# Performance work log

Hardware: AMD Instinct MI355X
Metric: run time of the kernel (lower is better)

Reference implementation:

```python
import jax, jax.numpy as jnp
import numpy as np

MIN_STD = 0.01
FOURIER_SCALE = 20.0


def _grid_sample_bilinear(h_flat, gx, gy):
    """Bilinear grid_sample with align_corners=True.
    h_flat: (N, C, H, W); gx, gy: (N, P) in [-1, 1].
    Returns (N, P, C)."""
    N, C, H, W = h_flat.shape
    x = (gx + 1.0) * 0.5 * (W - 1)
    y = (gy + 1.0) * 0.5 * (H - 1)
    x0 = jnp.clip(jnp.floor(x), 0, W - 1)
    y0 = jnp.clip(jnp.floor(y), 0, H - 1)
    x1 = jnp.clip(x0 + 1, 0, W - 1)
    y1 = jnp.clip(y0 + 1, 0, H - 1)
    wx = x - x0
    wy = y - y0
    x0i, x1i = x0.astype(jnp.int32), x1.astype(jnp.int32)
    y0i, y1i = y0.astype(jnp.int32), y1.astype(jnp.int32)
    hf = h_flat.reshape(N, C, H * W)  # flatten spatial for gather

    def gather(yi, xi):
        idx = (yi * W + xi)[:, None, :]  # (N,1,P)
        return jnp.take_along_axis(hf, idx, axis=2)  # (N,C,P)

    v00 = gather(y0i, x0i)
    v01 = gather(y0i, x1i)
    v10 = gather(y1i, x0i)
    v11 = gather(y1i, x1i)
    wx_ = wx[:, None, :]
    wy_ = wy[:, None, :]
    top = v00 * (1 - wx_) + v01 * wx_
    bot = v10 * (1 - wx_) + v11 * wx_
    out = top * (1 - wy_) + bot * wy_  # (N,C,P)
    return out.transpose(0, 2, 1)  # (N,P,C)


def setup_inputs() -> dict:
    key = jax.random.key(0)
    ks = jax.random.split(key, 9)
    B, T, C, Hg, Wg, P = 8, 16, 128, 64, 64, 2048
    h_dim, fmap = 128, 128
    in_dim = h_dim + 2 * fmap  # 384
    h_grid = jax.random.normal(ks[0], (B, T, C, Hg, Wg), dtype=jnp.float32)
    xs = jax.random.uniform(ks[1], (B, T, P, 1), dtype=jnp.float32)
    ys = jax.random.uniform(ks[2], (B, T, P, 1), dtype=jnp.float32)
    B_mat = jax.random.normal(ks[3], (2, fmap), dtype=jnp.float32) * FOURIER_SCALE
    W0 = jax.random.normal(ks[4], (in_dim, h_dim), dtype=jnp.float32) / np.sqrt(in_dim)
    b0 = jnp.zeros((h_dim,), dtype=jnp.float32)
    W1 = jax.random.normal(ks[5], (h_dim, h_dim), dtype=jnp.float32) / np.sqrt(h_dim)
    b1 = jnp.zeros((h_dim,), dtype=jnp.float32)
    W2 = jax.random.normal(ks[6], (h_dim, 2), dtype=jnp.float32) / np.sqrt(h_dim)
    b2 = jnp.zeros((2,), dtype=jnp.float32)
    return {"h_grid": h_grid, "xs": xs, "ys": ys, "B_mat": B_mat,
            "W0": W0, "b0": b0, "W1": W1, "b1": b1, "W2": W2, "b2": b2}


def reference(h_grid, xs, ys, B_mat, W0, b0, W1, b1, W2, b2):
    B, T, P, _ = xs.shape
    _, _, C, Hg, Wg = h_grid.shape
    h_flat = h_grid.reshape(B * T, C, Hg, Wg)
    coords = jnp.concatenate([xs, ys], axis=-1).reshape(B * T, P, 2)
    # map [spatial_min, spatial_max]=[0,1] to [-1,1]
    g = 2.0 * coords - 1.0
    sampled = _grid_sample_bilinear(h_flat, g[..., 0], g[..., 1])  # (BT,P,C)
    # Fourier features: [sin(2pi x B), cos(2pi x B)]
    proj = 2.0 * jnp.pi * jnp.einsum('npd,df->npf', coords, B_mat)
    spatial = jnp.concatenate([jnp.sin(proj), jnp.cos(proj)], axis=-1)  # (BT,P,256)
    x = jnp.concatenate([sampled, spatial], axis=-1)  # (BT,P,384)
    x = jax.nn.relu(x @ W0 + b0)
    x = jax.nn.relu(x @ W1 + b1)
    out = (x @ W2 + b2).reshape(B, T, P, 2)
    mu = out[..., 0:1]
    sigma = jax.nn.softplus(out[..., 1:2]) + MIN_STD
    return jnp.concatenate([mu, sigma], axis=-1)  # (B,T,P,2)
```

## Files before the change

kernel.cpp:

```cpp
#include <hip/hip_runtime.h>
#include <hip/hip_bf16.h>
#include <math.h>

typedef __attribute__((ext_vector_type(8))) short short8;
typedef __attribute__((ext_vector_type(4))) float f32x4;

__device__ __forceinline__ float b2f(unsigned short u) {
    union { unsigned int i; float f; } v; v.i = ((unsigned int)u) << 16; return v.f;
}
__device__ __forceinline__ unsigned short f2b(float f) {
    __hip_bfloat16 h = __float2bfloat16(f);
    return *reinterpret_cast<unsigned short*>(&h);
}

__global__ __launch_bounds__(256) void transpose_h(const float* __restrict__ hg,
                                                   unsigned short* __restrict__ ht) {
    __shared__ float t[64][65];
    int bid = blockIdx.x;
    int n  = bid >> 7;
    int cb = (bid >> 6) & 1;
    int pb = bid & 63;
    int tid = threadIdx.x;
    int j = tid & 63, i0 = tid >> 6;
    const float* src = hg + ((size_t)(n * 128 + cb * 64)) * 4096 + pb * 64;
#pragma unroll
    for (int ii = 0; ii < 16; ++ii) {
        int i = i0 + ii * 4;
        t[i][j] = src[(size_t)i * 4096 + j];
    }
    __syncthreads();
    int c = tid & 63, j0 = tid >> 6;
    unsigned short* dst = ht + ((size_t)n * 4096 + pb * 64) * 128 + cb * 64 + c;
#pragma unroll
    for (int jj = 0; jj < 16; ++jj) {
        int jr = j0 + jj * 4;
        dst[(size_t)jr * 128] = f2b(t[c][jr]);
    }
}

__global__ void prep_weights(const float* __restrict__ W0, const float* __restrict__ W1,
                             unsigned short* __restrict__ w0t, unsigned short* __restrict__ w1t) {
    int i = blockIdx.x * 256 + threadIdx.x;
    const int total0 = 128 * 384, total1 = 128 * 128;
    for (int idx = i; idx < total0; idx += gridDim.x * 256) {
        int j = idx / 384, k = idx - j * 384;
        w0t[idx] = f2b(W0[k * 128 + j]);
    }
    for (int idx = i; idx < total1; idx += gridDim.x * 256) {
        int j = idx >> 7, k = idx & 127;
        w1t[idx] = f2b(W1[k * 128 + j]);
    }
}

#define HSTR 136
#define MFMA_BF16 __builtin_amdgcn_mfma_f32_16x16x32_bf16

__device__ __forceinline__ const short8* w0frag(const unsigned short* w0s, int row, int kb) {
    return (const short8*)((const char*)w0s + row * 768 + (kb ^ ((row & 7) << 4)));
}

__global__ __launch_bounds__(512, 2) void fused_decoder(
    const unsigned short* __restrict__ ht,
    const float* __restrict__ xs, const float* __restrict__ ys,
    const float* __restrict__ Bm,
    const unsigned short* __restrict__ w0t, const float* __restrict__ b0,
    const unsigned short* __restrict__ w1t, const float* __restrict__ b1,
    const float* __restrict__ W2, const float* __restrict__ b2,
    float* __restrict__ out)
{
    __shared__ unsigned short w0s[128 * 384];
    __shared__ unsigned short hb_all[8 * 16 * HSTR];
    __shared__ unsigned short w2l[256];

    int tid = threadIdx.x, lane = tid & 63, w = tid >> 6;
    int lr = lane & 15, lg = lane >> 4;
    unsigned short* hb = hb_all + w * 16 * HSTR;

    {
        const short8* src = (const short8*)w0t;
#pragma unroll
        for (int it = 0; it < 12; ++it) {
            int c = tid + it * 512;
            int row = c / 48;
            int wb = (c - row * 48) * 16;
            short8 v = src[c];
            *(short8*)((char*)w0s + row * 768 + (wb ^ ((row & 7) << 4))) = v;
        }
        if (tid < 256) { int o = tid >> 7, k = tid & 127; w2l[o * 128 + k] = f2b(W2[k * 2 + o]); }
    }
    __syncthreads();

    int bid = blockIdx.x;
    int swz = (bid & 7) * 128 + (bid >> 3);
    int n = swz >> 3;
    int pbw = (swz & 7) * 256 + w * 32;
    int gp0 = n * 2048 + pbw;

    float xm[2], ym[2], wxv[2], wyv[2];
    int o00[2], o01[2], o10[2], o11[2];
#pragma unroll
    for (int m = 0; m < 2; ++m) {
        int gp = gp0 + m * 16 + lr;
        float x = xs[gp], y = ys[gp];
        xm[m] = x; ym[m] = y;
        float px = x * 63.f, py = y * 63.f;
        float x0f = fminf(fmaxf(floorf(px), 0.f), 63.f);
        float y0f = fminf(fmaxf(floorf(py), 0.f), 63.f);
        wxv[m] = px - x0f; wyv[m] = py - y0f;
        int xi0 = (int)x0f, yi0 = (int)y0f;
        int xi1 = min(xi0 + 1, 63), yi1 = min(yi0 + 1, 63);
        o00[m] = (yi0 * 64 + xi0) * 256;
        o01[m] = (yi0 * 64 + xi1) * 256;
        o10[m] = (yi1 * 64 + xi0) * 256;
        o11[m] = (yi1 * 64 + xi1) * 256;
    }
    const char* base = (const char*)ht + ((size_t)n << 20) + lg * 16;

    f32x4 acc[2][8];
#pragma unroll
    for (int nj = 0; nj < 8; ++nj) {
        float bv = b0[nj * 16 + lr];
        acc[0][nj] = (f32x4){bv, bv, bv, bv};
        acc[1][nj] = acc[0][nj];
    }

    short8 c00[2], c01[2], c10[2], c11[2];
#pragma unroll
    for (int m = 0; m < 2; ++m) {
        c00[m] = *(const short8*)(base + o00[m]);
        c01[m] = *(const short8*)(base + o01[m]);
        c10[m] = *(const short8*)(base + o10[m]);
        c11[m] = *(const short8*)(base + o11[m]);
    }

#pragma unroll
    for (int s = 0; s < 4; ++s) {
        int f0 = s * 32 + lg * 8;
        f32x4 B0a = *(const f32x4*)&Bm[f0];
        f32x4 B0b = *(const f32x4*)&Bm[f0 + 4];
        f32x4 B1a = *(const f32x4*)&Bm[128 + f0];
        f32x4 B1b = *(const f32x4*)&Bm[128 + f0 + 4];
        short8 asn[2], acs[2];
#pragma unroll
        for (int m = 0; m < 2; ++m) {
            float t_[8];
#pragma unroll
            for (int j = 0; j < 4; ++j) {
                t_[j]     = xm[m] * B0a[j] + ym[m] * B1a[j];
                t_[4 + j] = xm[m] * B0b[j] + ym[m] * B1b[j];
            }
#pragma unroll
            for (int j = 0; j < 8; ++j) {
                float tf = t_[j] - floorf(t_[j]);
                float sv, cv;
                asm("v_sin_f32 %0, %1" : "=v"(sv) : "v"(tf));
                asm("v_cos_f32 %0, %1" : "=v"(cv) : "v"(tf));
                asn[m][j] = (short)f2b(sv);
                acs[m][j] = (short)f2b(cv);
            }
        }
        int kbs = (4 + s) * 64 + lg * 16, kbc = (8 + s) * 64 + lg * 16;
#pragma unroll
        for (int nj = 0; nj < 8; ++nj) {
            short8 bs = *w0frag(w0s, nj * 16 + lr, kbs);
            acc[0][nj] = MFMA_BF16(asn[0], bs, acc[0][nj], 0, 0, 0);
            acc[1][nj] = MFMA_BF16(asn[1], bs, acc[1][nj], 0, 0, 0);
        }
#pragma unroll
        for (int nj = 0; nj < 8; ++nj) {
            short8 bc = *w0frag(w0s, nj * 16 + lr, kbc);
            acc[0][nj] = MFMA_BF16(acs[0], bc, acc[0][nj], 0, 0, 0);
            acc[1][nj] = MFMA_BF16(acs[1], bc, acc[1][nj], 0, 0, 0);
        }

        short8 a[2];
#pragma unroll
        for (int m = 0; m < 2; ++m) {
            float wx = wxv[m], wy = wyv[m];
            float ivx = 1.f - wx, ivy = 1.f - wy;
#pragma unroll
            for (int j = 0; j < 8; ++j) {
                float top = b2f((unsigned short)c00[m][j]) * ivx + b2f((unsigned short)c01[m][j]) * wx;
                float bot = b2f((unsigned short)c10[m][j]) * ivx + b2f((unsigned short)c11[m][j]) * wx;
                a[m][j] = (short)f2b(top * ivy + bot * wy);
            }
        }
        if (s < 3) {
            int so = (s + 1) * 64;
#pragma unroll
            for (int m = 0; m < 2; ++m) {
                c00[m] = *(const short8*)(base + o00[m] + so);
                c01[m] = *(const short8*)(base + o01[m] + so);
                c10[m] = *(const short8*)(base + o10[m] + so);
                c11[m] = *(const short8*)(base + o11[m] + so);
            }
        }
        int kba = s * 64 + lg * 16;
#pragma unroll
        for (int nj = 0; nj < 8; ++nj) {
            short8 b = *w0frag(w0s, nj * 16 + lr, kba);
            acc[0][nj] = MFMA_BF16(a[0], b, acc[0][nj], 0, 0, 0);
            acc[1][nj] = MFMA_BF16(a[1], b, acc[1][nj], 0, 0, 0);
        }
    }

    short8 a1[2][4];
#pragma unroll
    for (int m = 0; m < 2; ++m) {
#pragma unroll
        for (int nj = 0; nj < 8; ++nj)
#pragma unroll
            for (int r = 0; r < 4; ++r)
                hb[(lg * 4 + r) * HSTR + nj * 16 + lr] = f2b(fmaxf(acc[m][nj][r], 0.f));
        asm volatile("s_waitcnt lgkmcnt(0)" ::: "memory");
#pragma unroll
        for (int ks = 0; ks < 4; ++ks)
            a1[m][ks] = *(const short8*)&hb[lr * HSTR + ks * 32 + lg * 8];
        asm volatile("s_waitcnt lgkmcnt(0)" ::: "memory");
    }
#pragma unroll
    for (int nj = 0; nj < 8; ++nj) {
        float bv = b1[nj * 16 + lr];
        acc[0][nj] = (f32x4){bv, bv, bv, bv};
        acc[1][nj] = acc[0][nj];
    }
#pragma unroll
    for (int ks = 0; ks < 4; ++ks)
#pragma unroll
        for (int nj = 0; nj < 8; ++nj) {
            short8 b = *(const short8*)&w1t[(nj * 16 + lr) * 128 + ks * 32 + lg * 8];
            acc[0][nj] = MFMA_BF16(a1[0][ks], b, acc[0][nj], 0, 0, 0);
            acc[1][nj] = MFMA_BF16(a1[1][ks], b, acc[1][nj], 0, 0, 0);
        }

    float bb2 = (lr < 2) ? b2[lr] : 0.f;
#pragma unroll
    for (int m = 0; m < 2; ++m) {
#pragma unroll
        for (int nj = 0; nj < 8; ++nj)
#pragma unroll
            for (int r = 0; r < 4; ++r)
                hb[(lg * 4 + r) * HSTR + nj * 16 + lr] = f2b(fmaxf(acc[m][nj][r], 0.f));
        asm volatile("s_waitcnt lgkmcnt(0)" ::: "memory");
        f32x4 acc2 = (f32x4){bb2, bb2, bb2, bb2};
#pragma unroll
        for (int ks = 0; ks < 4; ++ks) {
            short8 a2 = *(const short8*)&hb[lr * HSTR + ks * 32 + lg * 8];
            short8 bz = (short8){0, 0, 0, 0, 0, 0, 0, 0};
            if (lr < 2) bz = *(const short8*)&w2l[lr * 128 + ks * 32 + lg * 8];
            acc2 = MFMA_BF16(a2, bz, acc2, 0, 0, 0);
        }
        asm volatile("s_waitcnt lgkmcnt(0)" ::: "memory");
        if (lr < 2) {
#pragma unroll
            for (int r = 0; r < 4; ++r) {
                int gp = gp0 + m * 16 + lg * 4 + r;
                float v = acc2[r];
                if (lr == 0) {
                    out[gp * 2] = v;
                } else {
                    float sp = (v > 20.f) ? v : log1pf(expf(v));
                    out[gp * 2 + 1] = sp + 0.01f;
                }
            }
        }
    }
}

extern "C" void kernel_launch(void* const* d_in, const int* in_sizes, int n_in,
                              void* d_out, int out_size, void* d_ws, size_t ws_size,
                              hipStream_t stream) {
    const float* h_grid = (const float*)d_in[0];
    const float* xs = (const float*)d_in[1];
    const float* ys = (const float*)d_in[2];
    const float* Bm = (const float*)d_in[3];
    const float* W0 = (const float*)d_in[4];
    const float* b0 = (const float*)d_in[5];
    const float* W1 = (const float*)d_in[6];
    const float* b1 = (const float*)d_in[7];
    const float* W2 = (const float*)d_in[8];
    const float* b2 = (const float*)d_in[9];
    float* out = (float*)d_out;

    unsigned short* ht  = (unsigned short*)d_ws;
    unsigned short* w0t = (unsigned short*)((char*)d_ws + 134217728ull);
    unsigned short* w1t = w0t + 128 * 384;

    hipLaunchKernelGGL(transpose_h, dim3(16384), dim3(256), 0, stream, h_grid, ht);
    hipLaunchKernelGGL(prep_weights, dim3(64), dim3(256), 0, stream, W0, W1, w0t, w1t);
    hipLaunchKernelGGL(fused_decoder, dim3(1024), dim3(512), 0, stream,
                       ht, xs, ys, Bm, w0t, b0, w1t, b1, W2, b2, out);
}
```

Before: 210.7 us.

## Vectorize transpose stores, pad W0 in LDS, double-buffer grid-sample corner loads

Result: faster. 198.8 us (-5.6%).

```diff
diff --git a/kernel.cpp b/kernel.cpp
--- a/kernel.cpp
+++ b/kernel.cpp
@@ -4,6 +4,7 @@
 
 typedef __attribute__((ext_vector_type(8))) short short8;
 typedef __attribute__((ext_vector_type(4))) float f32x4;
+typedef __attribute__((ext_vector_type(4))) unsigned short us4;
 
 __device__ __forceinline__ float b2f(unsigned short u) {
     union { unsigned int i; float f; } v; v.i = ((unsigned int)u) << 16; return v.f;
@@ -15,33 +16,35 @@
 
 __global__ __launch_bounds__(256) void transpose_h(const float* __restrict__ hg,
                                                    unsigned short* __restrict__ ht) {
-    __shared__ float t[64][65];
+    __shared__ float t[128][65];
     int bid = blockIdx.x;
-    int n  = bid >> 7;
-    int cb = (bid >> 6) & 1;
-    int pb = bid & 63;
+    int n = bid >> 6, pb = bid & 63;
     int tid = threadIdx.x;
+    const float* src = hg + (size_t)n * 128 * 4096 + pb * 64;
     int j = tid & 63, i0 = tid >> 6;
-    const float* src = hg + ((size_t)(n * 128 + cb * 64)) * 4096 + pb * 64;
-#pragma unroll
-    for (int ii = 0; ii < 16; ++ii) {
-        int i = i0 + ii * 4;
-        t[i][j] = src[(size_t)i * 4096 + j];
+#pragma unroll
+    for (int ii = 0; ii < 32; ++ii) {
+        int ch = ii * 4 + i0;
+        t[ch][j] = src[(size_t)ch * 4096 + j];
     }
     __syncthreads();
-    int c = tid & 63, j0 = tid >> 6;
-    unsigned short* dst = ht + ((size_t)n * 4096 + pb * 64) * 128 + cb * 64 + c;
-#pragma unroll
-    for (int jj = 0; jj < 16; ++jj) {
-        int jr = j0 + jj * 4;
-        dst[(size_t)jr * 128] = f2b(t[c][jr]);
+#pragma unroll
+    for (int it = 0; it < 8; ++it) {
+        int idx = tid + it * 256;
+        int px = idx >> 5, cq = idx & 31;
+        us4 o;
+#pragma unroll
+        for (int r = 0; r < 4; ++r) o[r] = f2b(t[cq * 4 + r][px]);
+        *(us4*)&ht[((size_t)n * 4096 + pb * 64 + px) * 128 + cq * 4] = o;
     }
 }
 
 __global__ void prep_weights(const float* __restrict__ W0, const float* __restrict__ W1,
-                             unsigned short* __restrict__ w0t, unsigned short* __restrict__ w1t) {
+                             const float* __restrict__ W2,
+                             unsigned short* __restrict__ w0t, unsigned short* __restrict__ w1t,
+                             unsigned short* __restrict__ w2p) {
     int i = blockIdx.x * 256 + threadIdx.x;
-    const int total0 = 128 * 384, total1 = 128 * 128;
+    const int total0 = 128 * 384, total1 = 128 * 128, total2 = 16 * 128;
     for (int idx = i; idx < total0; idx += gridDim.x * 256) {
         int j = idx / 384, k = idx - j * 384;
         w0t[idx] = f2b(W0[k * 128 + j]);
@@ -50,14 +53,15 @@
         int j = idx >> 7, k = idx & 127;
         w1t[idx] = f2b(W1[k * 128 + j]);
     }
-}
-
-#define HSTR 136
+    for (int idx = i; idx < total2; idx += gridDim.x * 256) {
+        int r = idx >> 7, k = idx & 127;
+        w2p[idx] = (r < 2) ? f2b(W2[k * 2 + r]) : (unsigned short)0;
+    }
+}
+
+#define W0P 784
+#define HBP 272
 #define MFMA_BF16 __builtin_amdgcn_mfma_f32_16x16x32_bf16
-
-__device__ __forceinline__ const short8* w0frag(const unsigned short* w0s, int row, int kb) {
-    return (const short8*)((const char*)w0s + row * 768 + (kb ^ ((row & 7) << 4)));
-}
 
 __global__ __launch_bounds__(512, 2) void fused_decoder(
     const unsigned short* __restrict__ ht,
@@ -65,45 +69,40 @@
     const float* __restrict__ Bm,
     const unsigned short* __restrict__ w0t, const float* __restrict__ b0,
     const unsigned short* __restrict__ w1t, const float* __restrict__ b1,
-    const float* __restrict__ W2, const float* __restrict__ b2,
+    const unsigned short* __restrict__ w2p, const float* __restrict__ b2,
     float* __restrict__ out)
 {
-    __shared__ unsigned short w0s[128 * 384];
-    __shared__ unsigned short hb_all[8 * 16 * HSTR];
-    __shared__ unsigned short w2l[256];
-
+    __shared__ char smem[128 * W0P + 8 * 16 * HBP];
+    char* w0s = smem;
     int tid = threadIdx.x, lane = tid & 63, w = tid >> 6;
     int lr = lane & 15, lg = lane >> 4;
-    unsigned short* hb = hb_all + w * 16 * HSTR;
+    char* hb = smem + 128 * W0P + w * 16 * HBP;
 
     {
         const short8* src = (const short8*)w0t;
-#pragma unroll
+#pragma unroll 1
         for (int it = 0; it < 12; ++it) {
             int c = tid + it * 512;
-            int row = c / 48;
-            int wb = (c - row * 48) * 16;
-            short8 v = src[c];
-            *(short8*)((char*)w0s + row * 768 + (wb ^ ((row & 7) << 4))) = v;
-        }
-        if (tid < 256) { int o = tid >> 7, k = tid & 127; w2l[o * 128 + k] = f2b(W2[k * 2 + o]); }
+            int row = c / 48, cc = c - row * 48;
+            *(short8*)(w0s + row * W0P + cc * 16) = src[c];
+        }
     }
     __syncthreads();
 
     int bid = blockIdx.x;
-    int swz = (bid & 7) * 128 + (bid >> 3);
-    int n = swz >> 3;
-    int pbw = (swz & 7) * 256 + w * 32;
-    int gp0 = n * 2048 + pbw;
+    int x = bid & 7, s = bid >> 3;
+    int n = x * 16 + (s >> 3);
+    int pt = s & 7;
+    int gp0 = n * 2048 + pt * 256 + w * 32;
 
     float xm[2], ym[2], wxv[2], wyv[2];
     int o00[2], o01[2], o10[2], o11[2];
 #pragma unroll
     for (int m = 0; m < 2; ++m) {
         int gp = gp0 + m * 16 + lr;
-        float x = xs[gp], y = ys[gp];
-        xm[m] = x; ym[m] = y;
-        float px = x * 63.f, py = y * 63.f;
+        float xc = xs[gp], yc = ys[gp];
+        xm[m] = xc; ym[m] = yc;
+        float px = xc * 63.f, py = yc * 63.f;
         float x0f = fminf(fmaxf(floorf(px), 0.f), 63.f);
         float y0f = fminf(fmaxf(floorf(py), 0.f), 63.f);
         wxv[m] = px - x0f; wyv[m] = py - y0f;
@@ -124,83 +123,153 @@
         acc[1][nj] = acc[0][nj];
     }
 
-    short8 c00[2], c01[2], c10[2], c11[2];
+    short8 A00[2], A01[2], A10[2], A11[2];
+    short8 B00[2], B01[2], B10[2], B11[2];
 #pragma unroll
     for (int m = 0; m < 2; ++m) {
-        c00[m] = *(const short8*)(base + o00[m]);
-        c01[m] = *(const short8*)(base + o01[m]);
-        c10[m] = *(const short8*)(base + o10[m]);
-        c11[m] = *(const short8*)(base + o11[m]);
-    }
-
-#pragma unroll
-    for (int s = 0; s < 4; ++s) {
-        int f0 = s * 32 + lg * 8;
-        f32x4 B0a = *(const f32x4*)&Bm[f0];
-        f32x4 B0b = *(const f32x4*)&Bm[f0 + 4];
-        f32x4 B1a = *(const f32x4*)&Bm[128 + f0];
-        f32x4 B1b = *(const f32x4*)&Bm[128 + f0 + 4];
-        short8 asn[2], acs[2];
-#pragma unroll
-        for (int m = 0; m < 2; ++m) {
-            float t_[8];
-#pragma unroll
-            for (int j = 0; j < 4; ++j) {
-                t_[j]     = xm[m] * B0a[j] + ym[m] * B1a[j];
-                t_[4 + j] = xm[m] * B0b[j] + ym[m] * B1b[j];
-            }
-#pragma unroll
-            for (int j = 0; j < 8; ++j) {
-                float tf = t_[j] - floorf(t_[j]);
-                float sv, cv;
-                asm("v_sin_f32 %0, %1" : "=v"(sv) : "v"(tf));
-                asm("v_cos_f32 %0, %1" : "=v"(cv) : "v"(tf));
-                asn[m][j] = (short)f2b(sv);
-                acs[m][j] = (short)f2b(cv);
-            }
-        }
-        int kbs = (4 + s) * 64 + lg * 16, kbc = (8 + s) * 64 + lg * 16;
-#pragma unroll
-        for (int nj = 0; nj < 8; ++nj) {
-            short8 bs = *w0frag(w0s, nj * 16 + lr, kbs);
-            acc[0][nj] = MFMA_BF16(asn[0], bs, acc[0][nj], 0, 0, 0);
-            acc[1][nj] = MFMA_BF16(asn[1], bs, acc[1][nj], 0, 0, 0);
-        }
-#pragma unroll
-        for (int nj = 0; nj < 8; ++nj) {
-            short8 bc = *w0frag(w0s, nj * 16 + lr, kbc);
-            acc[0][nj] = MFMA_BF16(acs[0], bc, acc[0][nj], 0, 0, 0);
-            acc[1][nj] = MFMA_BF16(acs[1], bc, acc[1][nj], 0, 0, 0);
-        }
-
-        short8 a[2];
-#pragma unroll
-        for (int m = 0; m < 2; ++m) {
-            float wx = wxv[m], wy = wyv[m];
-            float ivx = 1.f - wx, ivy = 1.f - wy;
-#pragma unroll
-            for (int j = 0; j < 8; ++j) {
-                float top = b2f((unsigned short)c00[m][j]) * ivx + b2f((unsigned short)c01[m][j]) * wx;
-                float bot = b2f((unsigned short)c10[m][j]) * ivx + b2f((unsigned short)c11[m][j]) * wx;
-                a[m][j] = (short)f2b(top * ivy + bot * wy);
-            }
-        }
-        if (s < 3) {
-            int so = (s + 1) * 64;
+        A00[m] = *(const short8*)(base + o00[m]);
+        A01[m] = *(const short8*)(base + o01[m]);
+        A10[m] = *(const short8*)(base + o10[m]);
+        A11[m] = *(const short8*)(base + o11[m]);
+        B00[m] = *(const short8*)(base + o00[m] + 64);
+        B01[m] = *(const short8*)(base + o01[m] + 64);
+        B10[m] = *(const short8*)(base + o10[m] + 64);
+        B11[m] = *(const short8*)(base + o11[m] + 64);
+    }
+
+#pragma unroll 1
+    for (int s2 = 0; s2 < 2; ++s2) {
+        {
+            int q = 2 * s2;
+            short8 asn[2], acs[2];
 #pragma unroll
             for (int m = 0; m < 2; ++m) {
-                c00[m] = *(const short8*)(base + o00[m] + so);
-                c01[m] = *(const short8*)(base + o01[m] + so);
-                c10[m] = *(const short8*)(base + o10[m] + so);
-                c11[m] = *(const short8*)(base + o11[m] + so);
-            }
-        }
-        int kba = s * 64 + lg * 16;
-#pragma unroll
-        for (int nj = 0; nj < 8; ++nj) {
-            short8 b = *w0frag(w0s, nj * 16 + lr, kba);
-            acc[0][nj] = MFMA_BF16(a[0], b, acc[0][nj], 0, 0, 0);
-            acc[1][nj] = MFMA_BF16(a[1], b, acc[1][nj], 0, 0, 0);
+                int f0 = q * 32 + lg * 8;
+                f32x4 B0a = *(const f32x4*)&Bm[f0];
+                f32x4 B0b = *(const f32x4*)&Bm[f0 + 4];
+                f32x4 B1a = *(const f32x4*)&Bm[128 + f0];
+                f32x4 B1b = *(const f32x4*)&Bm[128 + f0 + 4];
+                float t_[8];
+#pragma unroll
+                for (int j = 0; j < 4; ++j) {
+                    t_[j]     = xm[m] * B0a[j] + ym[m] * B1a[j];
+                    t_[4 + j] = xm[m] * B0b[j] + ym[m] * B1b[j];
+                }
+#pragma unroll
+                for (int j = 0; j < 8; ++j) {
+                    float tf = t_[j] - floorf(t_[j]);
+                    float sv, cv;
+                    asm("v_sin_f32 %0, %1" : "=v"(sv) : "v"(tf));
+                    asm("v_cos_f32 %0, %1" : "=v"(cv) : "v"(tf));
+                    asn[m][j] = (short)f2b(sv);
+                    acs[m][j] = (short)f2b(cv);
+                }
+            }
+#pragma unroll
+            for (int nj = 0; nj < 8; ++nj) {
+                short8 bs = *(const short8*)(w0s + (nj * 16 + lr) * W0P + (4 + q) * 64 + lg * 16);
+                acc[0][nj] = MFMA_BF16(asn[0], bs, acc[0][nj], 0, 0, 0);
+                acc[1][nj] = MFMA_BF16(asn[1], bs, acc[1][nj], 0, 0, 0);
+            }
+#pragma unroll
+            for (int nj = 0; nj < 8; ++nj) {
+                short8 bc = *(const short8*)(w0s + (nj * 16 + lr) * W0P + (8 + q) * 64 + lg * 16);
+                acc[0][nj] = MFMA_BF16(acs[0], bc, acc[0][nj], 0, 0, 0);
+                acc[1][nj] = MFMA_BF16(acs[1], bc, acc[1][nj], 0, 0, 0);
+            }
+            short8 a[2];
+#pragma unroll
+            for (int m = 0; m < 2; ++m) {
+                float wx = wxv[m], wy = wyv[m];
+                float ivx = 1.f - wx, ivy = 1.f - wy;
+#pragma unroll
+                for (int j = 0; j < 8; ++j) {
+                    float top = b2f((unsigned short)A00[m][j]) * ivx + b2f((unsigned short)A01[m][j]) * wx;
+                    float bot = b2f((unsigned short)A10[m][j]) * ivx + b2f((unsigned short)A11[m][j]) * wx;
+                    a[m][j] = (short)f2b(top * ivy + bot * wy);
+                }
+            }
+            if (s2 == 0) {
+#pragma unroll
+                for (int m = 0; m < 2; ++m) {
+                    A00[m] = *(const short8*)(base + o00[m] + 128);
+                    A01[m] = *(const short8*)(base + o01[m] + 128);
+                    A10[m] = *(const short8*)(base + o10[m] + 128);
+                    A11[m] = *(const short8*)(base + o11[m] + 128);
+                }
+            }
+#pragma unroll
+            for (int nj = 0; nj < 8; ++nj) {
+                short8 b = *(const short8*)(w0s + (nj * 16 + lr) * W0P + q * 64 + lg * 16);
+                acc[0][nj] = MFMA_BF16(a[0], b, acc[0][nj], 0, 0, 0);
+                acc[1][nj] = MFMA_BF16(a[1], b, acc[1][nj], 0, 0, 0);
+            }
+        }
+        {
+            int q = 2 * s2 + 1;
+            short8 asn[2], acs[2];
+#pragma unroll
+            for (int m = 0; m < 2; ++m) {
+                int f0 = q * 32 + lg * 8;
+                f32x4 B0a = *(const f32x4*)&Bm[f0];
+                f32x4 B0b = *(const f32x4*)&Bm[f0 + 4];
+                f32x4 B1a = *(const f32x4*)&Bm[128 + f0];
+                f32x4 B1b = *(const f32x4*)&Bm[128 + f0 + 4];
+                float t_[8];
+#pragma unroll
+                for (int j = 0; j < 4; ++j) {
+                    t_[j]     = xm[m] * B0a[j] + ym[m] * B1a[j];
+                    t_[4 + j] = xm[m] * B0b[j] + ym[m] * B1b[j];
+                }
+#pragma unroll
+                for (int j = 0; j < 8; ++j) {
+                    float tf = t_[j] - floorf(t_[j]);
+                    float sv, cv;
+                    asm("v_sin_f32 %0, %1" : "=v"(sv) : "v"(tf));
+                    asm("v_cos_f32 %0, %1" : "=v"(cv) : "v"(tf));
+                    asn[m][j] = (short)f2b(sv);
+                    acs[m][j] = (short)f2b(cv);
+                }
+            }
+#pragma unroll
+            for (int nj = 0; nj < 8; ++nj) {
+                short8 bs = *(const short8*)(w0s + (nj * 16 + lr) * W0P + (4 + q) * 64 + lg * 16);
+                acc[0][nj] = MFMA_BF16(asn[0], bs, acc[0][nj], 0, 0, 0);
+                acc[1][nj] = MFMA_BF16(asn[1], bs, acc[1][nj], 0, 0, 0);
+            }
+#pragma unroll
+            for (int nj = 0; nj < 8; ++nj) {
+                short8 bc = *(const short8*)(w0s + (nj * 16 + lr) * W0P + (8 + q) * 64 + lg * 16);
+                acc[0][nj] = MFMA_BF16(acs[0], bc, acc[0][nj], 0, 0, 0);
+                acc[1][nj] = MFMA_BF16(acs[1], bc, acc[1][nj], 0, 0, 0);
+            }
+            short8 a[2];
+#pragma unroll
+            for (int m = 0; m < 2; ++m) {
+                float wx = wxv[m], wy = wyv[m];
+                float ivx = 1.f - wx, ivy = 1.f - wy;
+#pragma unroll
+                for (int j = 0; j < 8; ++j) {
+                    float top = b2f((unsigned short)B00[m][j]) * ivx + b2f((unsigned short)B01[m][j]) * wx;
+                    float bot = b2f((unsigned short)B10[m][j]) * ivx + b2f((unsigned short)B11[m][j]) * wx;
+                    a[m][j] = (short)f2b(top * ivy + bot * wy);
+                }
+            }
+            if (s2 == 0) {
+#pragma unroll
+                for (int m = 0; m < 2; ++m) {
+                    B00[m] = *(const short8*)(base + o00[m] + 192);
+                    B01[m] = *(const short8*)(base + o01[m] + 192);
+                    B10[m] = *(const short8*)(base + o10[m] + 192);
+                    B11[m] = *(const short8*)(base + o11[m] + 192);
+                }
+            }
+#pragma unroll
+            for (int nj = 0; nj < 8; ++nj) {
+                short8 b = *(const short8*)(w0s + (nj * 16 + lr) * W0P + q * 64 + lg * 16);
+                acc[0][nj] = MFMA_BF16(a[0], b, acc[0][nj], 0, 0, 0);
+                acc[1][nj] = MFMA_BF16(a[1], b, acc[1][nj], 0, 0, 0);
+            }
         }
     }
 
@@ -210,12 +279,15 @@
 #pragma unroll
         for (int nj = 0; nj < 8; ++nj)
 #pragma unroll
-            for (int r = 0; r < 4; ++r)
-                hb[(lg * 4 + r) * HSTR + nj * 16 + lr] = f2b(fmaxf(acc[m][nj][r], 0.f));
+            for (int r = 0; r < 4; ++r) {
+                int row = lg * 4 + r;
+                *(unsigned short*)(hb + row * HBP + (nj * 16 + lr) * 2) =
+                    f2b(fmaxf(acc[m][nj][r], 0.f));
+            }
         asm volatile("s_waitcnt lgkmcnt(0)" ::: "memory");
 #pragma unroll
         for (int ks = 0; ks < 4; ++ks)
-            a1[m][ks] = *(const short8*)&hb[lr * HSTR + ks * 32 + lg * 8];
+            a1[m][ks] = *(const short8*)(hb + lr * HBP + ks * 64 + lg * 16);
         asm volatile("s_waitcnt lgkmcnt(0)" ::: "memory");
     }
 #pragma unroll
@@ -239,28 +311,30 @@
 #pragma unroll
         for (int nj = 0; nj < 8; ++nj)
 #pragma unroll
-            for (int r = 0; r < 4; ++r)
-                hb[(lg * 4 + r) * HSTR + nj * 16 + lr] = f2b(fmaxf(acc[m][nj][r], 0.f));
+            for (int r = 0; r < 4; ++r) {
+                int row = lg * 4 + r;
+                *(unsigned short*)(hb + row * HBP + (nj * 16 + lr) * 2) =
+                    f2b(fmaxf(acc[m][nj][r], 0.f));
+            }
         asm volatile("s_waitcnt lgkmcnt(0)" ::: "memory");
         f32x4 acc2 = (f32x4){bb2, bb2, bb2, bb2};
 #pragma unroll
         for (int ks = 0; ks < 4; ++ks) {
-            short8 a2 = *(const short8*)&hb[lr * HSTR + ks * 32 + lg * 8];
-            short8 bz = (short8){0, 0, 0, 0, 0, 0, 0, 0};
-            if (lr < 2) bz = *(const short8*)&w2l[lr * 128 + ks * 32 + lg * 8];
+            short8 a2 = *(const short8*)(hb + lr * HBP + ks * 64 + lg * 16);
+            short8 bz = *(const short8*)&w2p[lr * 128 + ks * 32 + lg * 8];
             acc2 = MFMA_BF16(a2, bz, acc2, 0, 0, 0);
         }
         asm volatile("s_waitcnt lgkmcnt(0)" ::: "memory");
         if (lr < 2) {
 #pragma unroll
             for (int r = 0; r < 4; ++r) {
-                int gp = gp0 + m * 16 + lg * 4 + r;
+                int gpo = gp0 + m * 16 + lg * 4 + r;
                 float v = acc2[r];
                 if (lr == 0) {
-                    out[gp * 2] = v;
+                    out[gpo * 2] = v;
                 } else {
                     float sp = (v > 20.f) ? v : log1pf(expf(v));
-                    out[gp * 2 + 1] = sp + 0.01f;
+                    out[gpo * 2 + 1] = sp + 0.01f;
                 }
             }
         }
@@ -285,9 +359,9 @@
     unsigned short* ht  = (unsigned short*)d_ws;
     unsigned short* w0t = (unsigned short*)((char*)d_ws + 134217728ull);
     unsigned short* w1t = w0t + 128 * 384;
-
-    hipLaunchKernelGGL(transpose_h, dim3(16384), dim3(256), 0, stream, h_grid, ht);
-    hipLaunchKernelGGL(prep_weights, dim3(64), dim3(256), 0, stream, W0, W1, w0t, w1t);
-    hipLaunchKernelGGL(fused_decoder, dim3(1024), dim3(512), 0, stream,
-                       ht, xs, ys, Bm, w0t, b0, w1t, b1, W2, b2, out);
-}
+    unsigned short* w2p = w1t + 128 * 128;
+
+    transpose_h<<<dim3(8192), dim3(256), 0, stream>>>(h_grid, ht);
+    prep_weights<<<dim3(64), dim3(256), 0, stream>>>(W0, W1, W2, w0t, w1t, w2p);
+    fused_decoder<<<dim3(1024), dim3(512), 0, stream>>>(ht, xs, ys, Bm, w0t, b0, w1t, b1, w2p, b2, out);
+}
```
